# Kernel tuning notes

Hardware: AMD Instinct MI355X
Metric: run time of the kernel (lower is better)

## Reference

```python
import jax, jax.numpy as jnp
import numpy as np

B, S, D, E, L = 8, 512, 768, 768, 4000

def setup_inputs() -> dict:
    key = jax.random.key(0)
    k1, k2, k3, k4 = jax.random.split(key, 4)
    last_hidden_state = jax.random.normal(k1, (B, S, D), dtype=jnp.float32)
    label_feat = jax.random.normal(k2, (L, E), dtype=jnp.float32)
    # nn.Linear(D, E): weight [E, D], bias [E]; xavier-ish scale
    W = jax.random.normal(k3, (E, D), dtype=jnp.float32) * (1.0 / np.sqrt(D))
    bias = jax.random.normal(k4, (E,), dtype=jnp.float32) * 0.01
    return {"last_hidden_state": last_hidden_state, "label_feat": label_feat, "W": W, "bias": bias}

def reference(last_hidden_state, label_feat, W, bias):
    # proj: tanh(Linear(last_hidden_state))  -> [B, S, E]
    proj = jnp.tanh(jnp.einsum('bsd,ed->bse', last_hidden_state, W) + bias)
    # scores: bmm(label_feat [B,L,E], proj^T [B,E,S]) -> [B, L, S]
    scores = jnp.einsum('le,bse->bls', label_feat, proj)
    # softmax over dim=1 (the LABEL dim), as in the original
    weights = jax.nn.softmax(scores, axis=1)
    # attn: bmm(weights [B,L,S], last_hidden_state [B,S,D]) -> [B, L, D]
    attn_output = jnp.einsum('bls,bsd->bld', weights, last_hidden_state)
    return (weights, attn_output)
```

## Files before the change

kernel.cpp:

```cpp
#include <hip/hip_runtime.h>
#include <hip/hip_bf16.h>
#include <cmath>

typedef __attribute__((ext_vector_type(8))) short short8;
typedef __attribute__((ext_vector_type(4))) float f32x4;

#define SM_CH 16
#define WCH   32

__device__ inline ushort f2bf(float x) {
    union { float f; unsigned u; } v; v.f = x;
    unsigned r = v.u + 0x7FFF + ((v.u >> 16) & 1);
    return (ushort)(r >> 16);
}

__device__ inline void split2(float x, ushort& hi, ushort& lo) {
    union { float f; unsigned u; } v; v.f = x;
    hi = (ushort)(v.u >> 16);
    union { float f; unsigned u; } h; h.u = v.u & 0xFFFF0000u;
    union { float f; unsigned u; } d; d.f = x - h.f;
    lo = (ushort)(d.u >> 16);
}

__device__ inline int swz(int row, int byte_in_row) {
    return row * 128 + (byte_in_row ^ ((row & 7) << 4));
}

__device__ inline void gload16(const void* g, void* lds) {
    __builtin_amdgcn_global_load_lds(
        (const __attribute__((address_space(1))) unsigned int*)g,
        (__attribute__((address_space(3))) unsigned int*)lds, 16, 0, 0);
}

__device__ inline void xcd_remap(int& bx, int& by, int& bz) {
    unsigned nx = gridDim.x, ny = gridDim.y;
    unsigned nwg = nx * ny * gridDim.z;
    unsigned id = blockIdx.x + nx * (blockIdx.y + ny * blockIdx.z);
    unsigned q = nwg >> 3;
    unsigned s = (id & 7) * q + (id >> 3);
    bx = s % nx; unsigned r = s / nx;
    by = r % ny; bz = r / ny;
}

__global__ __launch_bounds__(512, 2) void mfma_sc2(
    const ushort* __restrict__ AH, const ushort* __restrict__ AL,
    const ushort* __restrict__ BH, const ushort* __restrict__ BL,
    float* __restrict__ Cb, float* __restrict__ pmo, float* __restrict__ pso,
    int M, int N, long long sB, long long sC)
{
    extern __shared__ char smem[];
    const int K = 768;

    int bx, by, bz; xcd_remap(bx, by, bz);
    const int bm = bx * 256;
    const int bn = by * 256;
    const long long z = bz;

    const ushort* BHb = BH + z * sB;
    const ushort* BLb = BL + z * sB;

    const int t    = threadIdx.x;
    const int lane = t & 63;
    const int w    = t >> 6;
    const int wr   = w >> 2;
    const int wc   = w & 3;
    const int lrow = lane & 15;
    const int kg16 = (lane >> 4) * 16;

    const ushort* srcA[4]; const ushort* srcB[4]; int ldsO[4];
    #pragma unroll
    for (int i = 0; i < 4; ++i) {
        const int row  = w * 32 + i * 8 + (lane >> 3);
        const int q    = (lane & 7) ^ (row & 7);
        const int colo = (q & 3) * 8;
        srcA[i] = ((q < 4) ? AH : AL) + (long long)min(bm + row, M - 1) * K + colo;
        srcB[i] = ((q < 4) ? BHb : BLb) + (long long)(bn + row) * K + colo;
        ldsO[i] = w * 4096 + i * 1024;
    }

#define STAGE(k0_, cur_)                                                      \
    {                                                                         \
        _Pragma("unroll")                                                     \
        for (int i = 0; i < 4; ++i) {                                         \
            gload16(srcA[i] + (k0_), smem + (cur_) * 32768 + ldsO[i]);        \
            gload16(srcB[i] + (k0_), smem + 65536 + (cur_) * 32768 + ldsO[i]);\
        }                                                                     \
    }

    STAGE(0, 0);
    STAGE(32, 1);
    asm volatile("s_waitcnt vmcnt(8)" ::: "memory");
    __builtin_amdgcn_s_barrier();

    f32x4 acc[8][4] = {};

    for (int tt = 0; tt < 24; ++tt) {
        const int cur = tt & 1;
        const char* Ab = smem + cur * 32768;
        const char* Bb = smem + 65536 + cur * 32768;

        __builtin_amdgcn_s_setprio(1);
        short8 bh[4], bl[4];
        #pragma unroll
        for (int n = 0; n < 4; ++n) {
            bh[n] = *(const short8*)(Bb + swz(wc * 64 + n * 16 + lrow, kg16));
            bl[n] = *(const short8*)(Bb + swz(wc * 64 + n * 16 + lrow, 64 + kg16));
        }
        #pragma unroll
        for (int g = 0; g < 2; ++g) {
            short8 ah[4], al[4];
            #pragma unroll
            for (int m4 = 0; m4 < 4; ++m4) {
                const int r = wr * 128 + (g * 4 + m4) * 16 + lrow;
                ah[m4] = *(const short8*)(Ab + swz(r, kg16));
                al[m4] = *(const short8*)(Ab + swz(r, 64 + kg16));
            }
            #pragma unroll
            for (int m4 = 0; m4 < 4; ++m4)
                #pragma unroll
                for (int n = 0; n < 4; ++n) {
                    acc[g*4+m4][n] = __builtin_amdgcn_mfma_f32_16x16x32_bf16(
                        al[m4], bh[n], acc[g*4+m4][n], 0, 0, 0);
                    acc[g*4+m4][n] = __builtin_amdgcn_mfma_f32_16x16x32_bf16(
                        ah[m4], bl[n], acc[g*4+m4][n], 0, 0, 0);
                    acc[g*4+m4][n] = __builtin_amdgcn_mfma_f32_16x16x32_bf16(
                        ah[m4], bh[n], acc[g*4+m4][n], 0, 0, 0);
                }
        }
        __builtin_amdgcn_s_setprio(0);

        asm volatile("s_waitcnt lgkmcnt(0)" ::: "memory");
        __builtin_amdgcn_s_barrier();

        if (tt + 2 < 24) {
            STAGE((tt + 2) * 32, cur);
            asm volatile("s_waitcnt vmcnt(8)" ::: "memory");
        } else {
            asm volatile("s_waitcnt vmcnt(0)" ::: "memory");
        }
        __builtin_amdgcn_s_barrier();
    }
#undef STAGE

    float* C = Cb + z * sC;
    const int r0 = bm + wr * 128 + (lane >> 4) * 4;
    const int c0 = bn + wc * 64 + (lane & 15);
    #pragma unroll
    for (int n = 0; n < 4; ++n) {
        const int col = c0 + n * 16;
        #pragma unroll
        for (int mi = 0; mi < 8; ++mi) {
            #pragma unroll
            for (int r = 0; r < 4; ++r) {
                const int row = r0 + mi * 16 + r;
                if (row < M) C[(long long)row * N + col] = acc[mi][n][r];
            }
        }
    }

    __syncthreads();
    float* red = (float*)smem;
    const int slot = wr * 4 + (lane >> 4);
    const int colb = wc * 64 + (lane & 15);

    float lm[4];
    #pragma unroll
    for (int n = 0; n < 4; ++n) {
        float v = -INFINITY;
        #pragma unroll
        for (int mi = 0; mi < 8; ++mi)
            #pragma unroll
            for (int r = 0; r < 4; ++r)
                if (r0 + mi * 16 + r < M) v = fmaxf(v, acc[mi][n][r]);
        lm[n] = v;
    }
    #pragma unroll
    for (int n = 0; n < 4; ++n)
        red[(colb + n * 16) * 8 + slot] = lm[n];
    __syncthreads();
    float cm[4];
    #pragma unroll
    for (int n = 0; n < 4; ++n) {
        float v = -INFINITY;
        #pragma unroll
        for (int s8 = 0; s8 < 8; ++s8)
            v = fmaxf(v, red[(colb + n * 16) * 8 + s8]);
        cm[n] = v;
    }
    __syncthreads();
    float ls[4];
    #pragma unroll
    for (int n = 0; n < 4; ++n) {
        float sum = 0.f;
        #pragma unroll
        for (int mi = 0; mi < 8; ++mi)
            #pragma unroll
            for (int r = 0; r < 4; ++r)
                if (r0 + mi * 16 + r < M) sum += __expf(acc[mi][n][r] - cm[n]);
        ls[n] = sum;
    }
    #pragma unroll
    for (int n = 0; n < 4; ++n)
        red[(colb + n * 16) * 8 + slot] = ls[n];
    __syncthreads();
    if (slot == 0) {
        #pragma unroll
        for (int n = 0; n < 4; ++n) {
            float sum = 0.f;
            #pragma unroll
            for (int s8 = 0; s8 < 8; ++s8)
                sum += red[(colb + n * 16) * 8 + s8];
            const int col = bn + colb + n * 16;
            pmo[(z * SM_CH + bx) * N + col] = cm[n];
            pso[(z * SM_CH + bx) * N + col] = sum;
        }
    }
}

template<int ROWS, int KS>
__device__ inline void stage_plane(const ushort* __restrict__ src,
                                   char* plane, int t, int rbase, int rmax)
{
    #pragma unroll
    for (int s = 0; s < ROWS / 64; ++s) {
        const int row = s * 64 + (t >> 3);
        const int col = (((t & 7) * 16) ^ ((row & 7) << 4)) >> 1;
        const int gr  = min(rbase + row, rmax);
        gload16(src + (long long)gr * KS + col,
                plane + s * 8192 + (t >> 6) * 1024);
    }
}

__global__ __launch_bounds__(512, 2) void mfma_attn8(
    const ushort* __restrict__ A, const ushort* __restrict__ B,
    float* __restrict__ Cb, int M, int N,
    long long sA, long long sB, long long sC)
{
    extern __shared__ char smem[];
    constexpr int ABYTES = 128 * 128;
    constexpr int NT = 8, KS = 512;

    int bx, by, bz; xcd_remap(bx, by, bz);
    const int bm = bx * 128;
    const int bn = by * 256;
    const long long z = bz;

    const ushort* Ab_g = A + z * sA;
    const ushort* Bb_g = B + z * sB;

    const int t    = threadIdx.x;
    const int lane = t & 63;
    const int w    = t >> 6;
    const int wr   = w >> 2;
    const int wc   = w & 3;
    const int lrow = lane & 15;
    const int kg16 = (lane >> 4) * 16;

    stage_plane<128, KS>(Ab_g, smem, t, bm, M - 1);
    stage_plane<256, KS>(Bb_g, smem + 2 * ABYTES, t, bn, N - 1);
    stage_plane<128, KS>(Ab_g + 64, smem + ABYTES, t, bm, M - 1);
    stage_plane<256, KS>(Bb_g + 64, smem + 2 * ABYTES + 32768, t, bn, N - 1);
    asm volatile("s_waitcnt vmcnt(6)" ::: "memory");
    __builtin_amdgcn_s_barrier();

    f32x4 acc[4][4] = {};

    for (int tt = 0; tt < NT; ++tt) {
        const int cur = tt & 1;
        char* Ab = smem + cur * ABYTES;
        char* Bb = smem + 2 * ABYTES + cur * 32768;

        __builtin_amdgcn_s_setprio(1);
        short8 bf[4][2];
        #pragma unroll
        for (int n = 0; n < 4; ++n)
            #pragma unroll
            for (int ks = 0; ks < 2; ++ks)
                bf[n][ks] = *(const short8*)(Bb + swz(wc * 64 + n * 16 + lrow,
                                                      ks * 64 + kg16));
        #pragma unroll
        for (int q = 0; q < 2; ++q) {
            short8 af[2][2];
            #pragma unroll
            for (int mi = 0; mi < 2; ++mi)
                #pragma unroll
                for (int ks = 0; ks < 2; ++ks)
                    af[mi][ks] = *(const short8*)(Ab +
                        swz(wr * 64 + (q * 2 + mi) * 16 + lrow, ks * 64 + kg16));
            #pragma unroll
            for (int ks = 0; ks < 2; ++ks)
                #pragma unroll
                for (int mi = 0; mi < 2; ++mi)
                    #pragma unroll
                    for (int n = 0; n < 4; ++n)
                        acc[q * 2 + mi][n] = __builtin_amdgcn_mfma_f32_16x16x32_bf16(
                            af[mi][ks], bf[n][ks], acc[q * 2 + mi][n], 0, 0, 0);
        }
        __builtin_amdgcn_s_setprio(0);

        asm volatile("s_waitcnt lgkmcnt(0)" ::: "memory");
        __builtin_amdgcn_s_barrier();

        if (tt + 2 < NT) {
            stage_plane<128, KS>(Ab_g + (tt + 2) * 64, smem + cur * ABYTES,
                                 t, bm, M - 1);
            stage_plane<256, KS>(Bb_g + (tt + 2) * 64,
                                 smem + 2 * ABYTES + cur * 32768, t, bn, N - 1);
            asm volatile("s_waitcnt vmcnt(6)" ::: "memory");
        } else {
            asm volatile("s_waitcnt vmcnt(0)" ::: "memory");
        }
        __builtin_amdgcn_s_barrier();
    }

    float* C = Cb + z * sC;
    const int r0 = bm + wr * 64 + (lane >> 4) * 4;
    const int c0 = bn + wc * 64 + (lane & 15);
    #pragma unroll
    for (int n = 0; n < 4; ++n) {
        const int col = c0 + n * 16;
        #pragma unroll
        for (int mi = 0; mi < 4; ++mi) {
            #pragma unroll
            for (int r = 0; r < 4; ++r) {
                const int row = r0 + mi * 16 + r;
                if (row < M) C[(long long)row * N + col] = acc[mi][n][r];
            }
        }
    }
}

__global__ __launch_bounds__(256) void split_planes_kernel(
    const float* __restrict__ in, ushort* __restrict__ H,
    ushort* __restrict__ L, long long n4)
{
    long long i = (long long)blockIdx.x * 256 + threadIdx.x;
    if (i >= n4) return;
    float4 v = *(const float4*)(in + i * 4);
    ushort h[4], l[4];
    split2(v.x, h[0], l[0]); split2(v.y, h[1], l[1]);
    split2(v.z, h[2], l[2]); split2(v.w, h[3], l[3]);
    *(ushort4*)(H + i * 4) = *(ushort4*)h;
    *(ushort4*)(L + i * 4) = *(ushort4*)l;
}

__global__ __launch_bounds__(256) void mfma_proj(
    const float* __restrict__ Ab, const float* __restrict__ Bb,
    ushort* __restrict__ CH, ushort* __restrict__ CL,
    const float* __restrict__ bias, int M, int N, int K)
{
    extern __shared__ char smem[];
    char* Ah = smem;
    char* Al = smem + 16384;
    char* Bh = smem + 32768;
    char* Bl = smem + 49152;

    int bx, by, bz; xcd_remap(bx, by, bz);
    const int bm = bx * 128;
    const int bn = by * 128;

    const int t  = threadIdx.x;
    const int srow = t >> 1;
    const int skh  = (t & 1) * 32;
    const float* ap = Ab + (long long)min(bm + srow, M - 1) * K + skh;
    const float* bp = Bb + (long long)min(bn + srow, N - 1) * K + skh;

    const int lane = t & 63;
    const int w    = t >> 6;
    const int wm   = (w >> 1) * 64;
    const int wn   = (w & 1) * 64;
    const int lrow = lane & 15;
    const int kg16 = (lane >> 4) * 16;

    f32x4 acc[4][4] = {};

    for (int k0 = 0; k0 < K; k0 += 64) {
        #pragma unroll
        for (int j = 0; j < 4; ++j) {
            float xs[8];
            *(float4*)&xs[0] = *(const float4*)(ap + k0 + j * 8);
            *(float4*)&xs[4] = *(const float4*)(ap + k0 + j * 8 + 4);
            ushort oh[8], ol[8];
            #pragma unroll
            for (int i = 0; i < 8; ++i) split2(xs[i], oh[i], ol[i]);
            const int off = swz(srow, skh * 2 + j * 16);
            *(uint4*)(Ah + off) = *(uint4*)oh;
            *(uint4*)(Al + off) = *(uint4*)ol;
        }
        #pragma unroll
        for (int j = 0; j < 4; ++j) {
            float xs[8];
            *(float4*)&xs[0] = *(const float4*)(bp + k0 + j * 8);
            *(float4*)&xs[4] = *(const float4*)(bp + k0 + j * 8 + 4);
            ushort oh[8], ol[8];
            #pragma unroll
            for (int i = 0; i < 8; ++i) split2(xs[i], oh[i], ol[i]);
            const int off = swz(srow, skh * 2 + j * 16);
            *(uint4*)(Bh + off) = *(uint4*)oh;
            *(uint4*)(Bl + off) = *(uint4*)ol;
        }
        __syncthreads();

        #pragma unroll
        for (int kk = 0; kk < 2; ++kk) {
            short8 ah[4], al[4];
            #pragma unroll
            for (int mi = 0; mi < 4; ++mi) {
                const int off = swz(wm + mi * 16 + lrow, kk * 64 + kg16);
                ah[mi] = *(const short8*)(Ah + off);
                al[mi] = *(const short8*)(Al + off);
            }
            #pragma unroll
            for (int ni = 0; ni < 4; ++ni) {
                const int off = swz(wn + ni * 16 + lrow, kk * 64 + kg16);
                short8 bh = *(const short8*)(Bh + off);
                short8 bl = *(const short8*)(Bl + off);
                #pragma unroll
                for (int mi = 0; mi < 4; ++mi) {
                    acc[mi][ni] = __builtin_amdgcn_mfma_f32_16x16x32_bf16(al[mi], bh, acc[mi][ni], 0, 0, 0);
                    acc[mi][ni] = __builtin_amdgcn_mfma_f32_16x16x32_bf16(ah[mi], bl, acc[mi][ni], 0, 0, 0);
                    acc[mi][ni] = __builtin_amdgcn_mfma_f32_16x16x32_bf16(ah[mi], bh, acc[mi][ni], 0, 0, 0);
                }
            }
        }
        __syncthreads();
    }

    const int r0 = bm + wm + (lane >> 4) * 4;
    const int c0 = bn + wn + (lane & 15);
    #pragma unroll
    for (int ni = 0; ni < 4; ++ni) {
        const int col = c0 + ni * 16;
        const float bv = bias[col];
        #pragma unroll
        for (int mi = 0; mi < 4; ++mi) {
            #pragma unroll
            for (int r = 0; r < 4; ++r) {
                const int row = r0 + mi * 16 + r;
                if (row < M) {
                    float x = tanhf(acc[mi][ni][r] + bv);
                    ushort h, l;
                    split2(x, h, l);
                    CH[(long long)row * N + col] = h;
                    CL[(long long)row * N + col] = l;
                }
            }
        }
    }
}

__global__ __launch_bounds__(256) void transpose_bf16_kernel(
    const float* __restrict__ in, ushort* __restrict__ out, int S, int D)
{
    __shared__ float tile[32][33];
    const int b = blockIdx.z;
    const int s0 = blockIdx.x * 32, d0 = blockIdx.y * 32;
    const int tx = threadIdx.x & 31, ty = threadIdx.x >> 5;
    const float* ip = in + (long long)b * S * D;
    #pragma unroll
    for (int i = 0; i < 32; i += 8)
        tile[ty + i][tx] = ip[(long long)(s0 + ty + i) * D + d0 + tx];
    __syncthreads();
    ushort* op = out + (long long)b * S * D;
    #pragma unroll
    for (int i = 0; i < 32; i += 8)
        op[(long long)(d0 + ty + i) * S + s0 + tx] = f2bf(tile[tx][ty + i]);
}

__global__ __launch_bounds__(256) void softmax_write2_kernel(
    float* __restrict__ scores, const float* __restrict__ pm,
    const float* __restrict__ ps, int L, int S, int chlen,
    ushort* __restrict__ wbf)
{
    int s = blockIdx.x * 256 + threadIdx.x;
    int c = blockIdx.y;
    int b = blockIdx.z;

    float m = -INFINITY;
    #pragma unroll
    for (int k = 0; k < SM_CH; ++k)
        m = fmaxf(m, pm[(b * SM_CH + k) * S + s]);
    float sum = 0.f;
    #pragma unroll
    for (int k = 0; k < SM_CH; ++k)
        sum += ps[(b * SM_CH + k) * S + s] * __expf(pm[(b * SM_CH + k) * S + s] - m);
    float inv = 1.f / sum;

    float* p = scores + (long long)b * L * S + s;
    ushort* q = wbf + (long long)b * L * S + s;
    int l0 = c * chlen;
    int l1 = min(L, l0 + chlen);
    for (int l = l0; l < l1; ++l) {
        float x = p[(long long)l * S];
        float v = __expf(x - m) * inv;
        p[(long long)l * S] = v;
        q[(long long)l * S] = f2bf(v);
    }
}

extern "C" void kernel_launch(void* const* d_in, const int* in_sizes, int n_in,
                              void* d_out, int out_size, void* d_ws, size_t ws_size,
                              hipStream_t stream)
{
    const int Bn = 8, S = 512, D = 768, E = 768, L = 4000;
    const float* lhs   = (const float*)d_in[0];
    const float* label = (const float*)d_in[1];
    const float* W     = (const float*)d_in[2];
    const float* bias  = (const float*)d_in[3];

    float* weights = (float*)d_out;
    float* attn    = (float*)d_out + (long long)Bn * L * S;

    const long long nLE  = (long long)L * E;
    const long long nBSE = (long long)Bn * S * E;
    const long long nBDS = (long long)Bn * D * S;
    const long long nBLS = (long long)Bn * L * S;

    ushort* labelH = (ushort*)d_ws;
    ushort* labelL = labelH + nLE;
    ushort* projH  = labelL + nLE;
    ushort* projL  = projH + nBSE;
    ushort* lhsT   = projL + nBSE;
    ushort* wbf    = lhsT + nBDS;
    float*  pm     = (float*)(wbf + nBLS);
    float*  ps     = pm + Bn * SM_CH * S;

    hipFuncSetAttribute((const void*)mfma_sc2,
                        hipFuncAttributeMaxDynamicSharedMemorySize, 131072);
    hipFuncSetAttribute((const void*)mfma_attn8,
                        hipFuncAttributeMaxDynamicSharedMemorySize, 98304);

    transpose_bf16_kernel<<<dim3(S / 32, D / 32, Bn), 256, 0, stream>>>(
        lhs, lhsT, S, D);
    split_planes_kernel<<<(int)(nLE / 4 + 255) / 256, 256, 0, stream>>>(
        label, labelH, labelL, nLE / 4);

    mfma_proj<<<dim3((Bn * S) / 128, E / 128, 1), 256, 65536, stream>>>(
        lhs, W, projH, projL, bias, Bn * S, E, D);

    mfma_sc2<<<dim3((L + 255) / 256, S / 256, Bn), 512, 131072, stream>>>(
        labelH, labelL, projH, projL, weights, pm, ps,
        L, S, (long long)S * E, (long long)L * S);

    softmax_write2_kernel<<<dim3(S / 256, WCH, Bn), 256, 0, stream>>>(
        weights, pm, ps, L, S, (L + WCH - 1) / WCH, wbf);

    mfma_attn8<<<dim3((L + 127) / 128, D / 256, Bn), 512, 98304, stream>>>(
        wbf, lhsT, attn, L, D,
        (long long)L * S, (long long)D * S, (long long)L * D);
}
```

Measured before the change: 243.9 us.

## Use 256x128 score tiles with triple-buffered LDS and split MFMA phases

Changes the scores GEMM tile from 256x256 to 256x128, giving 8 waves as a 4x2 layout and doubling the grid along S. It moves from double to triple-buffered LDS staging with prefetch depth 3, and splits each k-step into two half-phases separated by barriers so LDS reads and MFMA work interleave across waves. The aim is more blocks for occupancy and better latency hiding. The costs are more barriers, 144KB of LDS per block, which likely limits residency to one block per CU, and a larger cross-wave softmax reduction (16 slots).

```diff
diff --git a/kernel.cpp b/kernel.cpp
--- a/kernel.cpp
+++ b/kernel.cpp
@@ -42,7 +42,7 @@
     by = r % ny; bz = r / ny;
 }
 
-__global__ __launch_bounds__(512, 2) void mfma_sc2(
+__global__ __launch_bounds__(512, 2) void mfma_sc4(
     const ushort* __restrict__ AH, const ushort* __restrict__ AL,
     const ushort* __restrict__ BH, const ushort* __restrict__ BL,
     float* __restrict__ Cb, float* __restrict__ pmo, float* __restrict__ pso,
@@ -50,10 +50,11 @@
 {
     extern __shared__ char smem[];
     const int K = 768;
+    constexpr int NT = 24;
 
     int bx, by, bz; xcd_remap(bx, by, bz);
     const int bm = bx * 256;
-    const int bn = by * 256;
+    const int bn = by * 128;
     const long long z = bz;
 
     const ushort* BHb = BH + z * sB;
@@ -62,98 +63,136 @@
     const int t    = threadIdx.x;
     const int lane = t & 63;
     const int w    = t >> 6;
-    const int wr   = w >> 2;
-    const int wc   = w & 3;
+    const int wr   = w >> 1;
+    const int wc   = w & 1;
     const int lrow = lane & 15;
     const int kg16 = (lane >> 4) * 16;
 
-    const ushort* srcA[4]; const ushort* srcB[4]; int ldsO[4];
+    const int q    = (t & 7) ^ ((t >> 3) & 7);
+    const int colo = (q & 3) * 8;
+    const ushort* srcA[4]; const ushort* srcB[2];
+    int aldsO[4], bldsO[2];
     #pragma unroll
     for (int i = 0; i < 4; ++i) {
-        const int row  = w * 32 + i * 8 + (lane >> 3);
-        const int q    = (lane & 7) ^ (row & 7);
-        const int colo = (q & 3) * 8;
+        const int row = i * 64 + (t >> 3);
         srcA[i] = ((q < 4) ? AH : AL) + (long long)min(bm + row, M - 1) * K + colo;
+        aldsO[i] = i * 8192 + w * 1024;
+    }
+    #pragma unroll
+    for (int i = 0; i < 2; ++i) {
+        const int row = i * 64 + (t >> 3);
         srcB[i] = ((q < 4) ? BHb : BLb) + (long long)(bn + row) * K + colo;
-        ldsO[i] = w * 4096 + i * 1024;
-    }
-
-#define STAGE(k0_, cur_)                                                      \
+        bldsO[i] = i * 8192 + w * 1024;
+    }
+
+#define STAGE(tile_, r_)                                                      \
     {                                                                         \
+        const int kk_ = (tile_) * 32;                                         \
         _Pragma("unroll")                                                     \
-        for (int i = 0; i < 4; ++i) {                                         \
-            gload16(srcA[i] + (k0_), smem + (cur_) * 32768 + ldsO[i]);        \
-            gload16(srcB[i] + (k0_), smem + 65536 + (cur_) * 32768 + ldsO[i]);\
-        }                                                                     \
+        for (int i = 0; i < 4; ++i)                                           \
+            gload16(srcA[i] + kk_, smem + (r_) * 32768 + aldsO[i]);           \
+        _Pragma("unroll")                                                     \
+        for (int i = 0; i < 2; ++i)                                           \
+            gload16(srcB[i] + kk_, smem + 98304 + (r_) * 16384 + bldsO[i]);   \
     }
 
     STAGE(0, 0);
-    STAGE(32, 1);
-    asm volatile("s_waitcnt vmcnt(8)" ::: "memory");
+    STAGE(1, 1);
+    STAGE(2, 2);
+    asm volatile("s_waitcnt vmcnt(12)" ::: "memory");
     __builtin_amdgcn_s_barrier();
 
-    f32x4 acc[8][4] = {};
-
-    for (int tt = 0; tt < 24; ++tt) {
-        const int cur = tt & 1;
-        const char* Ab = smem + cur * 32768;
-        const char* Bb = smem + 65536 + cur * 32768;
-
-        __builtin_amdgcn_s_setprio(1);
+    f32x4 acc[4][4] = {};
+    int r = 0;
+
+    for (int tt = 0; tt < NT; ++tt) {
+        const char* Ab = smem + r * 32768;
+        const char* Bb = smem + 98304 + r * 16384;
+
         short8 bh[4], bl[4];
         #pragma unroll
         for (int n = 0; n < 4; ++n) {
-            bh[n] = *(const short8*)(Bb + swz(wc * 64 + n * 16 + lrow, kg16));
-            bl[n] = *(const short8*)(Bb + swz(wc * 64 + n * 16 + lrow, 64 + kg16));
-        }
-        #pragma unroll
-        for (int g = 0; g < 2; ++g) {
-            short8 ah[4], al[4];
-            #pragma unroll
-            for (int m4 = 0; m4 < 4; ++m4) {
-                const int r = wr * 128 + (g * 4 + m4) * 16 + lrow;
-                ah[m4] = *(const short8*)(Ab + swz(r, kg16));
-                al[m4] = *(const short8*)(Ab + swz(r, 64 + kg16));
-            }
-            #pragma unroll
-            for (int m4 = 0; m4 < 4; ++m4)
+            const int br = wc * 64 + n * 16 + lrow;
+            bh[n] = *(const short8*)(Bb + swz(br, kg16));
+            bl[n] = *(const short8*)(Bb + swz(br, 64 + kg16));
+        }
+        {
+            short8 ah[2], al[2];
+            #pragma unroll
+            for (int m = 0; m < 2; ++m) {
+                const int ar = wr * 64 + m * 16 + lrow;
+                ah[m] = *(const short8*)(Ab + swz(ar, kg16));
+                al[m] = *(const short8*)(Ab + swz(ar, 64 + kg16));
+            }
+            __builtin_amdgcn_s_barrier();
+            asm volatile("s_waitcnt lgkmcnt(0)" ::: "memory");
+            __builtin_amdgcn_s_setprio(1);
+            #pragma unroll
+            for (int m = 0; m < 2; ++m)
                 #pragma unroll
                 for (int n = 0; n < 4; ++n) {
-                    acc[g*4+m4][n] = __builtin_amdgcn_mfma_f32_16x16x32_bf16(
-                        al[m4], bh[n], acc[g*4+m4][n], 0, 0, 0);
-                    acc[g*4+m4][n] = __builtin_amdgcn_mfma_f32_16x16x32_bf16(
-                        ah[m4], bl[n], acc[g*4+m4][n], 0, 0, 0);
-                    acc[g*4+m4][n] = __builtin_amdgcn_mfma_f32_16x16x32_bf16(
-                        ah[m4], bh[n], acc[g*4+m4][n], 0, 0, 0);
+                    acc[m][n] = __builtin_amdgcn_mfma_f32_16x16x32_bf16(
+                        al[m], bh[n], acc[m][n], 0, 0, 0);
+                    acc[m][n] = __builtin_amdgcn_mfma_f32_16x16x32_bf16(
+                        ah[m], bl[n], acc[m][n], 0, 0, 0);
+                    acc[m][n] = __builtin_amdgcn_mfma_f32_16x16x32_bf16(
+                        ah[m], bh[n], acc[m][n], 0, 0, 0);
                 }
-        }
-        __builtin_amdgcn_s_setprio(0);
-
-        asm volatile("s_waitcnt lgkmcnt(0)" ::: "memory");
+            __builtin_amdgcn_s_setprio(0);
+            __builtin_amdgcn_s_barrier();
+        }
+
+        {
+            short8 ah[2], al[2];
+            #pragma unroll
+            for (int m = 0; m < 2; ++m) {
+                const int ar = wr * 64 + (m + 2) * 16 + lrow;
+                ah[m] = *(const short8*)(Ab + swz(ar, kg16));
+                al[m] = *(const short8*)(Ab + swz(ar, 64 + kg16));
+            }
+            __builtin_amdgcn_s_barrier();
+            asm volatile("s_waitcnt lgkmcnt(0)" ::: "memory");
+            __builtin_amdgcn_s_setprio(1);
+            #pragma unroll
+            for (int m = 0; m < 2; ++m)
+                #pragma unroll
+                for (int n = 0; n < 4; ++n) {
+                    acc[m + 2][n] = __builtin_amdgcn_mfma_f32_16x16x32_bf16(
+                        al[m], bh[n], acc[m + 2][n], 0, 0, 0);
+                    acc[m + 2][n] = __builtin_amdgcn_mfma_f32_16x16x32_bf16(
+                        ah[m], bl[n], acc[m + 2][n], 0, 0, 0);
+                    acc[m + 2][n] = __builtin_amdgcn_mfma_f32_16x16x32_bf16(
+                        ah[m], bh[n], acc[m + 2][n], 0, 0, 0);
+                }
+            __builtin_amdgcn_s_setprio(0);
+            __builtin_amdgcn_s_barrier();
+        }
+
+        if (tt + 3 < NT) {
+            STAGE(tt + 3, r);
+            asm volatile("s_waitcnt vmcnt(12)" ::: "memory");
+        } else if (tt + 3 == NT) {
+            asm volatile("s_waitcnt vmcnt(6)" ::: "memory");
+        } else if (tt + 2 == NT) {
+            asm volatile("s_waitcnt vmcnt(0)" ::: "memory");
+        }
         __builtin_amdgcn_s_barrier();
-
-        if (tt + 2 < 24) {
-            STAGE((tt + 2) * 32, cur);
-            asm volatile("s_waitcnt vmcnt(8)" ::: "memory");
-        } else {
-            asm volatile("s_waitcnt vmcnt(0)" ::: "memory");
-        }
-        __builtin_amdgcn_s_barrier();
+        r = (r == 2) ? 0 : r + 1;
     }
 #undef STAGE
 
     float* C = Cb + z * sC;
-    const int r0 = bm + wr * 128 + (lane >> 4) * 4;
+    const int r0 = bm + wr * 64 + (lane >> 4) * 4;
     const int c0 = bn + wc * 64 + (lane & 15);
     #pragma unroll
     for (int n = 0; n < 4; ++n) {
         const int col = c0 + n * 16;
         #pragma unroll
-        for (int mi = 0; mi < 8; ++mi) {
-            #pragma unroll
-            for (int r = 0; r < 4; ++r) {
-                const int row = r0 + mi * 16 + r;
-                if (row < M) C[(long long)row * N + col] = acc[mi][n][r];
+        for (int mi = 0; mi < 4; ++mi) {
+            #pragma unroll
+            for (int rr = 0; rr < 4; ++rr) {
+                const int row = r0 + mi * 16 + rr;
+                if (row < M) C[(long long)row * N + col] = acc[mi][n][rr];
             }
         }
     }
@@ -168,23 +207,23 @@
     for (int n = 0; n < 4; ++n) {
         float v = -INFINITY;
         #pragma unroll
-        for (int mi = 0; mi < 8; ++mi)
-            #pragma unroll
-            for (int r = 0; r < 4; ++r)
-                if (r0 + mi * 16 + r < M) v = fmaxf(v, acc[mi][n][r]);
+        for (int mi = 0; mi < 4; ++mi)
+            #pragma unroll
+            for (int rr = 0; rr < 4; ++rr)
+                if (r0 + mi * 16 + rr < M) v = fmaxf(v, acc[mi][n][rr]);
         lm[n] = v;
     }
     #pragma unroll
     for (int n = 0; n < 4; ++n)
-        red[(colb + n * 16) * 8 + slot] = lm[n];
+        red[(colb + n * 16) * 16 + slot] = lm[n];
     __syncthreads();
     float cm[4];
     #pragma unroll
     for (int n = 0; n < 4; ++n) {
         float v = -INFINITY;
         #pragma unroll
-        for (int s8 = 0; s8 < 8; ++s8)
-            v = fmaxf(v, red[(colb + n * 16) * 8 + s8]);
+        for (int s16 = 0; s16 < 16; ++s16)
+            v = fmaxf(v, red[(colb + n * 16) * 16 + s16]);
         cm[n] = v;
     }
     __syncthreads();
@@ -193,23 +232,23 @@
     for (int n = 0; n < 4; ++n) {
         float sum = 0.f;
         #pragma unroll
-        for (int mi = 0; mi < 8; ++mi)
-            #pragma unroll
-            for (int r = 0; r < 4; ++r)
-                if (r0 + mi * 16 + r < M) sum += __expf(acc[mi][n][r] - cm[n]);
+        for (int mi = 0; mi < 4; ++mi)
+            #pragma unroll
+            for (int rr = 0; rr < 4; ++rr)
+                if (r0 + mi * 16 + rr < M) sum += __expf(acc[mi][n][rr] - cm[n]);
         ls[n] = sum;
     }
     #pragma unroll
     for (int n = 0; n < 4; ++n)
-        red[(colb + n * 16) * 8 + slot] = ls[n];
+        red[(colb + n * 16) * 16 + slot] = ls[n];
     __syncthreads();
     if (slot == 0) {
         #pragma unroll
         for (int n = 0; n < 4; ++n) {
             float sum = 0.f;
             #pragma unroll
-            for (int s8 = 0; s8 < 8; ++s8)
-                sum += red[(colb + n * 16) * 8 + s8];
+            for (int s16 = 0; s16 < 16; ++s16)
+                sum += red[(colb + n * 16) * 16 + s16];
             const int col = bn + colb + n * 16;
             pmo[(z * SM_CH + bx) * N + col] = cm[n];
             pso[(z * SM_CH + bx) * N + col] = sum;
@@ -525,8 +564,8 @@
     float*  pm     = (float*)(wbf + nBLS);
     float*  ps     = pm + Bn * SM_CH * S;
 
-    hipFuncSetAttribute((const void*)mfma_sc2,
-                        hipFuncAttributeMaxDynamicSharedMemorySize, 131072);
+    hipFuncSetAttribute((const void*)mfma_sc4,
+                        hipFuncAttributeMaxDynamicSharedMemorySize, 147456);
     hipFuncSetAttribute((const void*)mfma_attn8,
                         hipFuncAttributeMaxDynamicSharedMemorySize, 98304);
 
@@ -538,7 +577,7 @@
     mfma_proj<<<dim3((Bn * S) / 128, E / 128, 1), 256, 65536, stream>>>(
         lhs, W, projH, projL, bias, Bn * S, E, D);
 
-    mfma_sc2<<<dim3((L + 255) / 256, S / 256, Bn), 512, 131072, stream>>>(
+    mfma_sc4<<<dim3((L + 255) / 256, S / 128, Bn), 512, 147456, stream>>>(
         labelH, labelL, projH, projL, weights, pm, ps,
         L, S, (long long)S * E, (long long)L * S);
 
```

Result: slower. 263.5 us (+8.0%).
